# Kernel tuning notes

Measured on AMD Instinct MI355X. Metric: run time of the kernel, lower is better.

## Reference

```python
import jax, jax.numpy as jnp
import numpy as np

DIM = 1024
CTX_DIM = 1024
HEADS = 8
DIM_HEAD = 64
INNER = HEADS * DIM_HEAD  # 512
EPS = 1e-5


def _layer_norm(x, gamma, beta):
    mu = jnp.mean(x, axis=-1, keepdims=True)
    var = jnp.mean(jnp.square(x - mu), axis=-1, keepdims=True)
    return (x - mu) * jax.lax.rsqrt(var + EPS) * gamma + beta


def setup_inputs() -> dict:
    key = jax.random.key(0)
    ks = jax.random.split(key, 8)
    b, n, m = 4, 2048, 2048
    x = jax.random.normal(ks[0], (b, n, DIM), dtype=jnp.float32)
    context = jax.random.normal(ks[1], (b, m, CTX_DIM), dtype=jnp.float32)
    Wq = jax.random.normal(ks[2], (DIM, INNER), dtype=jnp.float32) / np.sqrt(DIM)
    Wkv = jax.random.normal(ks[3], (CTX_DIM, 2 * INNER), dtype=jnp.float32) / np.sqrt(CTX_DIM)
    Wout = jax.random.normal(ks[4], (INNER, DIM), dtype=jnp.float32) / np.sqrt(INNER)
    bout = jnp.zeros((DIM,), dtype=jnp.float32)
    g1 = jnp.ones((DIM,), dtype=jnp.float32)
    b1 = jnp.zeros((DIM,), dtype=jnp.float32)
    g2 = jnp.ones((CTX_DIM,), dtype=jnp.float32)
    b2 = jnp.zeros((CTX_DIM,), dtype=jnp.float32)
    return {"x": x, "context": context, "g1": g1, "b1": b1, "g2": g2, "b2": b2,
            "Wq": Wq, "Wkv": Wkv, "Wout": Wout, "bout": bout}


def reference(x, context, g1, b1, g2, b2, Wq, Wkv, Wout, bout):
    b, n, _ = x.shape
    m = context.shape[1]
    scale = DIM_HEAD ** -0.5
    xn = _layer_norm(x, g1, b1)
    cn = _layer_norm(context, g2, b2)
    q = xn @ Wq                      # [b, n, inner]
    kv = cn @ Wkv                    # [b, m, 2*inner]
    k, v = jnp.split(kv, 2, axis=-1)
    # split heads: [b, h, seq, d]
    q = q.reshape(b, n, HEADS, DIM_HEAD).transpose(0, 2, 1, 3)
    k = k.reshape(b, m, HEADS, DIM_HEAD).transpose(0, 2, 1, 3)
    v = v.reshape(b, m, HEADS, DIM_HEAD).transpose(0, 2, 1, 3)
    sim = jnp.einsum('bhid,bhjd->bhij', q, k) * scale
    attn = jax.nn.softmax(sim, axis=-1)
    out = jnp.einsum('bhij,bhjd->bhid', attn, v)
    out = out.transpose(0, 2, 1, 3).reshape(b, n, INNER)
    return out @ Wout + bout
```

## Files before the change

kernel.cpp:

```cpp
#include <hip/hip_runtime.h>
#include <hip/hip_bf16.h>

typedef __bf16 bf16_t;
typedef bf16_t bf16x4 __attribute__((ext_vector_type(4)));
typedef bf16_t bf16x8 __attribute__((ext_vector_type(8)));
typedef float floatx4 __attribute__((ext_vector_type(4)));

typedef __attribute__((address_space(1))) const unsigned char* gptr_t;
typedef __attribute__((address_space(3))) unsigned char* lptr_t;

#define BATCH 4
#define SEQ_N 2048
#define SEQ_M 2048
#define DIM 1024
#define INNER 512
#define HEADS 8
#define DHEAD 64
#define QSCALE 0.18033688011112042f

__device__ __forceinline__ void wtrans_tile(const float* W, bf16_t* Wt,
                                            int K, int N, int n0, int k0, float scale) {
    __shared__ bf16_t T[64][72];
    const int tid = threadIdx.x;
#pragma unroll
    for (int p = 0; p < 2; p++) {
        int r = (tid >> 3) + p * 32;
        int c = (tid & 7) * 8;
        const float* src = W + (size_t)(k0 + r) * N + n0 + c;
        float4 v0 = *(const float4*)src;
        float4 v1 = *(const float4*)(src + 4);
        T[r][c + 0] = (bf16_t)(v0.x * scale); T[r][c + 1] = (bf16_t)(v0.y * scale);
        T[r][c + 2] = (bf16_t)(v0.z * scale); T[r][c + 3] = (bf16_t)(v0.w * scale);
        T[r][c + 4] = (bf16_t)(v1.x * scale); T[r][c + 5] = (bf16_t)(v1.y * scale);
        T[r][c + 6] = (bf16_t)(v1.z * scale); T[r][c + 7] = (bf16_t)(v1.w * scale);
    }
    __syncthreads();
#pragma unroll
    for (int p = 0; p < 2; p++) {
        int rn = (tid >> 3) + p * 32;
        int ck = (tid & 7) * 8;
        bf16x8 v;
#pragma unroll
        for (int i = 0; i < 8; i++) v[i] = T[ck + i][rn];
        *(bf16x8*)(Wt + (size_t)(n0 + rn) * K + k0 + ck) = v;
    }
}

__device__ __forceinline__ void ln_row_wave(const float* in, const float* g,
                                            const float* bt, bf16_t* out, int row) {
    const int lane = threadIdx.x & 63;
    const float4* src = (const float4*)(in + (size_t)row * 1024);
    float4 xv[4];
    float s = 0.f, ss = 0.f;
#pragma unroll
    for (int k = 0; k < 4; k++) {
        xv[k] = src[lane + k * 64];
        s  += xv[k].x + xv[k].y + xv[k].z + xv[k].w;
        ss += xv[k].x * xv[k].x + xv[k].y * xv[k].y + xv[k].z * xv[k].z + xv[k].w * xv[k].w;
    }
#pragma unroll
    for (int off = 32; off > 0; off >>= 1) {
        s  += __shfl_down(s, off);
        ss += __shfl_down(ss, off);
    }
    s  = __shfl(s, 0);
    ss = __shfl(ss, 0);
    const float mu = s * (1.f / 1024.f);
    const float var = ss * (1.f / 1024.f) - mu * mu;
    const float rs = rsqrtf(var + 1e-5f);
    const float4* gp = (const float4*)g;
    const float4* bp = (const float4*)bt;
#pragma unroll
    for (int k = 0; k < 4; k++) {
        float4 gv = gp[lane + k * 64], bv = bp[lane + k * 64];
        bf16x4 o;
        o[0] = (bf16_t)((xv[k].x - mu) * rs * gv.x + bv.x);
        o[1] = (bf16_t)((xv[k].y - mu) * rs * gv.y + bv.y);
        o[2] = (bf16_t)((xv[k].z - mu) * rs * gv.z + bv.z);
        o[3] = (bf16_t)((xv[k].w - mu) * rs * gv.w + bv.w);
        *(bf16x4*)(out + (size_t)row * 1024 + (lane + k * 64) * 4) = o;
    }
}

__global__ __launch_bounds__(256) void prep_kernel(const float* __restrict__ x,
                                                   const float* __restrict__ ctx,
                                                   const float* __restrict__ g1,
                                                   const float* __restrict__ b1,
                                                   const float* __restrict__ g2,
                                                   const float* __restrict__ b2,
                                                   const float* __restrict__ Wq,
                                                   const float* __restrict__ Wkv,
                                                   const float* __restrict__ Wout,
                                                   bf16_t* __restrict__ xn,
                                                   bf16_t* __restrict__ cn,
                                                   bf16_t* __restrict__ Wqt,
                                                   bf16_t* __restrict__ Wkvt,
                                                   bf16_t* __restrict__ Woutt) {
    int id = blockIdx.x;
    if (id < 128) {
        wtrans_tile(Wq, Wqt, 1024, 512, (id & 7) * 64, (id >> 3) * 64, QSCALE);
    } else if (id < 384) {
        int t = id - 128;
        wtrans_tile(Wkv, Wkvt, 1024, 1024, (t & 15) * 64, (t >> 4) * 64, 1.0f);
    } else if (id < 512) {
        int t = id - 384;
        wtrans_tile(Wout, Woutt, 512, 1024, (t & 15) * 64, (t >> 4) * 64, 1.0f);
    } else {
        int row = (id - 512) * 4 + (threadIdx.x >> 6);
        if (row < BATCH * SEQ_N) ln_row_wave(x, g1, b1, xn, row);
        else                     ln_row_wave(ctx, g2, b2, cn, row - BATCH * SEQ_N);
    }
}

template <int NT, int MODE, typename OutT>
__device__ __forceinline__ void gemm_body(const bf16_t* __restrict__ A,
                                          const bf16_t* __restrict__ Bt,
                                          OutT* __restrict__ C,
                                          const float* __restrict__ bias,
                                          int ldC, int K, int row0, int col0) {
    __shared__ bf16_t As[128 * 64];
    __shared__ bf16_t Bs[NT * 64];
    const int tid = threadIdx.x;
    const int wave = tid >> 6, lane = tid & 63;
    constexpr int WC = NT / 2;
    constexpr int NJ = WC / 16;
    const int wr = (wave >> 1) * 64, wc = (wave & 1) * WC;
    const int quad = lane >> 4, l16 = lane & 15;

    floatx4 acc[4][NJ] = {};

    for (int k0 = 0; k0 < K; k0 += 64) {
#pragma unroll
        for (int p = 0; p < 4; p++) {
            int cA = p * 256 + wave * 64 + lane;
            int rA = cA >> 3, kc = (cA & 7) * 8;
            __builtin_amdgcn_global_load_lds(
                (gptr_t)(A + (size_t)(row0 + rA) * K + k0 + kc),
                (lptr_t)(As + (size_t)(p * 256 + wave * 64) * 8), 16, 0, 0);
            if (p < NT / 32)
                __builtin_amdgcn_global_load_lds(
                    (gptr_t)(Bt + (size_t)(col0 + rA) * K + k0 + kc),
                    (lptr_t)(Bs + (size_t)(p * 256 + wave * 64) * 8), 16, 0, 0);
        }
        __syncthreads();
#pragma unroll
        for (int kt = 0; kt < 2; kt++) {
            bf16x8 aF[4], bF[NJ];
#pragma unroll
            for (int i = 0; i < 4; i++)
                aF[i] = *(bf16x8*)&As[(wr + i * 16 + l16) * 64 + kt * 32 + quad * 8];
#pragma unroll
            for (int j = 0; j < NJ; j++)
                bF[j] = *(bf16x8*)&Bs[(wc + j * 16 + l16) * 64 + kt * 32 + quad * 8];
#pragma unroll
            for (int i = 0; i < 4; i++)
#pragma unroll
                for (int j = 0; j < NJ; j++) {
                    if (MODE == 0)
                        acc[i][j] = __builtin_amdgcn_mfma_f32_16x16x32_bf16(
                            aF[i], bF[j], acc[i][j], 0, 0, 0);
                    else
                        acc[i][j] = __builtin_amdgcn_mfma_f32_16x16x32_bf16(
                            bF[j], aF[i], acc[i][j], 0, 0, 0);
                }
        }
        __syncthreads();
    }

    if (MODE == 0) {
#pragma unroll
        for (int i = 0; i < 4; i++)
#pragma unroll
            for (int j = 0; j < NJ; j++) {
                int col = col0 + wc + j * 16 + l16;
                float bv = bias ? bias[col] : 0.f;
#pragma unroll
                for (int r = 0; r < 4; r++) {
                    int row = row0 + wr + i * 16 + quad * 4 + r;
                    C[(size_t)row * ldC + col] = (OutT)(acc[i][j][r] + bv);
                }
            }
    } else {
        bf16_t* Tw = (wave < 2 ? As : Bs) + (wave & 1) * 4096;
#pragma unroll
        for (int i = 0; i < 4; i++)
#pragma unroll
            for (int j = 0; j < 4; j++)
#pragma unroll
                for (int r = 0; r < 4; r++)
                    Tw[(j * 16 + quad * 4 + r) * 64 + i * 16 + l16] = (bf16_t)acc[i][j][r];
        __syncthreads();
        const int grow = row0 + wr;
        const int bat = grow >> 11, gm = (grow & 2047) + l16 * 4;
#pragma unroll
        for (int dd = 0; dd < 16; dd++) {
            int d = dd * 4 + quad;
            bf16x4 v = *(bf16x4*)&Tw[d * 64 + l16 * 4];
            int gd = col0 + wc + d - 512;
            *(bf16x4*)(C + ((size_t)bat * 512 + gd) * 2048 + gm) = v;
        }
    }
}

__global__ __launch_bounds__(256) void gemm_qkv_kernel(const bf16_t* __restrict__ xn,
                                                       const bf16_t* __restrict__ cn,
                                                       const bf16_t* __restrict__ Wqt,
                                                       const bf16_t* __restrict__ Wkvt,
                                                       bf16_t* __restrict__ qb,
                                                       bf16_t* __restrict__ kvb,
                                                       bf16_t* __restrict__ Vtg) {
    const int bx = blockIdx.x;
    const int row0 = blockIdx.y * 128;
    if (bx < 4)
        gemm_body<128, 0, bf16_t>(xn, Wqt, qb, nullptr, 512, DIM, row0, bx * 128);
    else if (bx < 8)
        gemm_body<128, 0, bf16_t>(cn, Wkvt, kvb, nullptr, 512, DIM, row0, (bx - 4) * 128);
    else
        gemm_body<128, 1, bf16_t>(cn, Wkvt, Vtg, nullptr, 0, DIM, row0, (bx - 4) * 128);
}

__global__ __launch_bounds__(256) void gemm_out_kernel(const bf16_t* __restrict__ ao,
                                                       const bf16_t* __restrict__ Woutt,
                                                       float* __restrict__ out,
                                                       const float* __restrict__ bias) {
    gemm_body<64, 0, float>(ao, Woutt, out, bias, DIM, INNER,
                            blockIdx.y * 128, blockIdx.x * 64);
}

#define PSTR 72
__global__ __launch_bounds__(256) void attn_kernel(const bf16_t* __restrict__ q,
                                                   const bf16_t* __restrict__ kv,
                                                   const bf16_t* __restrict__ Vtg,
                                                   bf16_t* __restrict__ o) {
    __shared__ bf16_t Qs[64 * 72];
    __shared__ bf16_t Ks[64 * 72];
    __shared__ bf16_t Vs[64 * 72];

    const int b = blockIdx.z, h = blockIdx.y;
    const int n0 = blockIdx.x * 64;
    const int tid = threadIdx.x;
    const int wave = tid >> 6, lane = tid & 63;
    const int quad = lane >> 4, l16 = lane & 15;

    const int sr = (tid >> 3);
    const int sc = (tid & 7) * 8;

#pragma unroll
    for (int p = 0; p < 2; p++) {
        int r = sr + p * 32;
        *(bf16x8*)&Qs[r * 72 + sc] =
            *(const bf16x8*)(q + (size_t)(b * SEQ_N + n0 + r) * INNER + h * DHEAD + sc);
    }

    bf16x8 bOnes;
    {
        bf16_t ov = (l16 == 0) ? (bf16_t)1.0f : (bf16_t)0.0f;
#pragma unroll
        for (int i = 0; i < 8; i++) bOnes[i] = ov;
    }

    const bf16_t* kp = kv + (size_t)(b * SEQ_M) * 512 + h * DHEAD + sc;
    const bf16_t* vp = Vtg + (size_t)((b * HEADS + h) * DHEAD) * SEQ_M + sc;
    bf16x8 kreg[2], vreg[2];
#pragma unroll
    for (int p = 0; p < 2; p++) {
        kreg[p] = *(const bf16x8*)(kp + (size_t)(sr + p * 32) * 512);
        vreg[p] = *(const bf16x8*)(vp + (size_t)(sr + p * 32) * SEQ_M);
    }
    __syncthreads();

    bf16x8 aQ[2];
#pragma unroll
    for (int kt = 0; kt < 2; kt++)
        aQ[kt] = *(bf16x8*)&Qs[(wave * 16 + l16) * 72 + kt * 32 + quad * 8];

    bf16_t* Pw = Qs + wave * (16 * PSTR);

    floatx4 oacc[5] = {};

    for (int it = 0; it < SEQ_M / 64; ++it) {
        __syncthreads();
#pragma unroll
        for (int p = 0; p < 2; p++) {
            int r = sr + p * 32;
            *(bf16x8*)&Ks[r * 72 + sc] = kreg[p];
            *(bf16x8*)&Vs[r * 72 + sc] = vreg[p];
        }
        __syncthreads();

        kp += 64 * 512;
        vp += 64;
#pragma unroll
        for (int p = 0; p < 2; p++) {
            kreg[p] = *(const bf16x8*)(kp + (size_t)(sr + p * 32) * 512);
            vreg[p] = *(const bf16x8*)(vp + (size_t)(sr + p * 32) * SEQ_M);
        }

        floatx4 s[4] = {};
#pragma unroll
        for (int kt = 0; kt < 2; kt++)
#pragma unroll
            for (int jt = 0; jt < 4; jt++) {
                bf16x8 aK = *(bf16x8*)&Ks[(jt * 16 + l16) * 72 + kt * 32 + quad * 8];
                s[jt] = __builtin_amdgcn_mfma_f32_16x16x32_bf16(aK, aQ[kt], s[jt], 0, 0, 0);
            }

#pragma unroll
        for (int jt = 0; jt < 4; jt++) {
            bf16x4 pk;
#pragma unroll
            for (int r = 0; r < 4; r++) pk[r] = (bf16_t)exp2f(s[jt][r]);
            *(bf16x4*)&Pw[l16 * PSTR + jt * 16 + quad * 4] = pk;
        }

#pragma unroll
        for (int kt = 0; kt < 2; kt++) {
            bf16x8 aP = *(bf16x8*)&Pw[l16 * PSTR + kt * 32 + quad * 8];
#pragma unroll
            for (int dt = 0; dt < 4; dt++) {
                bf16x8 bV = *(bf16x8*)&Vs[(dt * 16 + l16) * 72 + kt * 32 + quad * 8];
                oacc[dt] = __builtin_amdgcn_mfma_f32_16x16x32_bf16(aP, bV, oacc[dt], 0, 0, 0);
            }
            oacc[4] = __builtin_amdgcn_mfma_f32_16x16x32_bf16(aP, bOnes, oacc[4], 0, 0, 0);
        }
    }

    float inv[4];
#pragma unroll
    for (int r = 0; r < 4; r++) {
        float l = __shfl(oacc[4][r], (int)(lane & 48));
        inv[r] = 1.0f / l;
    }
#pragma unroll
    for (int dt = 0; dt < 4; dt++)
#pragma unroll
        for (int r = 0; r < 4; r++) {
            int row = n0 + wave * 16 + quad * 4 + r;
            int col = h * DHEAD + dt * 16 + l16;
            o[(size_t)(b * SEQ_N + row) * INNER + col] =
                (bf16_t)(oacc[dt][r] * inv[r]);
        }
}

extern "C" void kernel_launch(void* const* d_in, const int* in_sizes, int n_in,
                              void* d_out, int out_size, void* d_ws, size_t ws_size,
                              hipStream_t stream) {
    const float* x    = (const float*)d_in[0];
    const float* ctx  = (const float*)d_in[1];
    const float* g1   = (const float*)d_in[2];
    const float* b1   = (const float*)d_in[3];
    const float* g2   = (const float*)d_in[4];
    const float* b2   = (const float*)d_in[5];
    const float* Wq   = (const float*)d_in[6];
    const float* Wkv  = (const float*)d_in[7];
    const float* Wout = (const float*)d_in[8];
    const float* bout = (const float*)d_in[9];
    float* out = (float*)d_out;

    const int rows = BATCH * SEQ_N;
    bf16_t* xn    = (bf16_t*)d_ws;
    bf16_t* cn    = xn + (size_t)rows * DIM;
    bf16_t* qb    = cn + (size_t)rows * DIM;
    bf16_t* kvb   = qb + (size_t)rows * INNER;
    bf16_t* Vtg   = kvb + (size_t)rows * INNER;
    bf16_t* Wqt   = Vtg + (size_t)rows * INNER;
    bf16_t* Wkvt  = Wqt + (size_t)INNER * DIM;
    bf16_t* Woutt = Wkvt + (size_t)(2 * INNER) * DIM;
    bf16_t* o_attn = xn;

    prep_kernel<<<512 + (2 * rows) / 4, 256, 0, stream>>>(
        x, ctx, g1, b1, g2, b2, Wq, Wkv, Wout, xn, cn, Wqt, Wkvt, Woutt);
    gemm_qkv_kernel<<<dim3(12, rows / 128), 256, 0, stream>>>(
        xn, cn, Wqt, Wkvt, qb, kvb, Vtg);
    attn_kernel<<<dim3(SEQ_N / 64, HEADS, BATCH), 256, 0, stream>>>(qb, kvb, Vtg, o_attn);
    gemm_out_kernel<<<dim3(DIM / 64, rows / 128), 256, 0, stream>>>(o_attn, Woutt, out, bout);
}
```

Before: 259.9 us.

## Double-buffer K/V, process two query tiles per wave, swizzle LDS in attention

Result: no change. 257.4 us (-0.9%).

```diff
diff --git a/kernel.cpp b/kernel.cpp
--- a/kernel.cpp
+++ b/kernel.cpp
@@ -227,28 +227,32 @@
                             blockIdx.y * 128, blockIdx.x * 64);
 }
 
-#define PSTR 72
-__global__ __launch_bounds__(256) void attn_kernel(const bf16_t* __restrict__ q,
+__global__ __launch_bounds__(128) void attn_kernel(const bf16_t* __restrict__ q,
                                                    const bf16_t* __restrict__ kv,
                                                    const bf16_t* __restrict__ Vtg,
                                                    bf16_t* __restrict__ o) {
-    __shared__ bf16_t Qs[64 * 72];
-    __shared__ bf16_t Ks[64 * 72];
-    __shared__ bf16_t Vs[64 * 72];
-
-    const int b = blockIdx.z, h = blockIdx.y;
-    const int n0 = blockIdx.x * 64;
+    __shared__ bf16_t Qs[64 * 64];
+    __shared__ bf16_t Ks[2][64 * 64];
+    __shared__ bf16_t Vs[2][64 * 64];
+
+    const int f = blockIdx.x;
+    const int lb = ((f & 7) << 7) | (f >> 3);
+    const int b = lb >> 8, h = (lb >> 5) & 7;
+    const int n0 = (lb & 31) * 64;
+
     const int tid = threadIdx.x;
     const int wave = tid >> 6, lane = tid & 63;
     const int quad = lane >> 4, l16 = lane & 15;
-
-    const int sr = (tid >> 3);
+    const int swz = (l16 & 7) << 3;
+
+    const int sr = tid >> 3;
     const int sc = (tid & 7) * 8;
-
-#pragma unroll
-    for (int p = 0; p < 2; p++) {
-        int r = sr + p * 32;
-        *(bf16x8*)&Qs[r * 72 + sc] =
+    const int scs = sc ^ ((sr & 7) << 3);
+
+#pragma unroll
+    for (int p = 0; p < 4; p++) {
+        int r = sr + p * 16;
+        *(bf16x8*)&Qs[r * 64 + scs] =
             *(const bf16x8*)(q + (size_t)(b * SEQ_N + n0 + r) * INNER + h * DHEAD + sc);
     }
 
@@ -261,85 +265,118 @@
 
     const bf16_t* kp = kv + (size_t)(b * SEQ_M) * 512 + h * DHEAD + sc;
     const bf16_t* vp = Vtg + (size_t)((b * HEADS + h) * DHEAD) * SEQ_M + sc;
-    bf16x8 kreg[2], vreg[2];
-#pragma unroll
-    for (int p = 0; p < 2; p++) {
-        kreg[p] = *(const bf16x8*)(kp + (size_t)(sr + p * 32) * 512);
-        vreg[p] = *(const bf16x8*)(vp + (size_t)(sr + p * 32) * SEQ_M);
+    bf16x8 kreg[4], vreg[4];
+#pragma unroll
+    for (int p = 0; p < 4; p++) {
+        kreg[p] = *(const bf16x8*)(kp + (size_t)(sr + p * 16) * 512);
+        vreg[p] = *(const bf16x8*)(vp + (size_t)(sr + p * 16) * SEQ_M);
     }
     __syncthreads();
 
-    bf16x8 aQ[2];
-#pragma unroll
-    for (int kt = 0; kt < 2; kt++)
-        aQ[kt] = *(bf16x8*)&Qs[(wave * 16 + l16) * 72 + kt * 32 + quad * 8];
-
-    bf16_t* Pw = Qs + wave * (16 * PSTR);
-
-    floatx4 oacc[5] = {};
-
+    bf16x8 aQ0[2], aQ1[2];
+#pragma unroll
+    for (int kt = 0; kt < 2; kt++) {
+        aQ0[kt] = *(bf16x8*)&Qs[(wave * 32 + l16) * 64 + ((kt * 32 + quad * 8) ^ swz)];
+        aQ1[kt] = *(bf16x8*)&Qs[(wave * 32 + 16 + l16) * 64 + ((kt * 32 + quad * 8) ^ swz)];
+    }
+
+#pragma unroll
+    for (int p = 0; p < 4; p++) {
+        int r = sr + p * 16;
+        *(bf16x8*)&Ks[0][r * 64 + scs] = kreg[p];
+        *(bf16x8*)&Vs[0][r * 64 + scs] = vreg[p];
+    }
+    kp += 64 * 512;
+    vp += 64;
+#pragma unroll
+    for (int p = 0; p < 4; p++) {
+        kreg[p] = *(const bf16x8*)(kp + (size_t)(sr + p * 16) * 512);
+        vreg[p] = *(const bf16x8*)(vp + (size_t)(sr + p * 16) * SEQ_M);
+    }
+    __syncthreads();
+
+    bf16_t* Pw0 = Qs + wave * 2048;
+    bf16_t* Pw1 = Pw0 + 1024;
+
+    floatx4 oacc0[5] = {}, oacc1[5] = {};
+
+    int cur = 0;
     for (int it = 0; it < SEQ_M / 64; ++it) {
-        __syncthreads();
-#pragma unroll
-        for (int p = 0; p < 2; p++) {
-            int r = sr + p * 32;
-            *(bf16x8*)&Ks[r * 72 + sc] = kreg[p];
-            *(bf16x8*)&Vs[r * 72 + sc] = vreg[p];
-        }
-        __syncthreads();
-
+#pragma unroll
+        for (int p = 0; p < 4; p++) {
+            int r = sr + p * 16;
+            *(bf16x8*)&Ks[cur ^ 1][r * 64 + scs] = kreg[p];
+            *(bf16x8*)&Vs[cur ^ 1][r * 64 + scs] = vreg[p];
+        }
         kp += 64 * 512;
         vp += 64;
 #pragma unroll
-        for (int p = 0; p < 2; p++) {
-            kreg[p] = *(const bf16x8*)(kp + (size_t)(sr + p * 32) * 512);
-            vreg[p] = *(const bf16x8*)(vp + (size_t)(sr + p * 32) * SEQ_M);
-        }
-
-        floatx4 s[4] = {};
+        for (int p = 0; p < 4; p++) {
+            kreg[p] = *(const bf16x8*)(kp + (size_t)(sr + p * 16) * 512);
+            vreg[p] = *(const bf16x8*)(vp + (size_t)(sr + p * 16) * SEQ_M);
+        }
+
+        floatx4 s0[4] = {}, s1[4] = {};
 #pragma unroll
         for (int kt = 0; kt < 2; kt++)
 #pragma unroll
             for (int jt = 0; jt < 4; jt++) {
-                bf16x8 aK = *(bf16x8*)&Ks[(jt * 16 + l16) * 72 + kt * 32 + quad * 8];
-                s[jt] = __builtin_amdgcn_mfma_f32_16x16x32_bf16(aK, aQ[kt], s[jt], 0, 0, 0);
+                bf16x8 aK = *(bf16x8*)&Ks[cur][(jt * 16 + l16) * 64 +
+                                              ((kt * 32 + quad * 8) ^ swz)];
+                s0[jt] = __builtin_amdgcn_mfma_f32_16x16x32_bf16(aK, aQ0[kt], s0[jt], 0, 0, 0);
+                s1[jt] = __builtin_amdgcn_mfma_f32_16x16x32_bf16(aK, aQ1[kt], s1[jt], 0, 0, 0);
             }
 
 #pragma unroll
         for (int jt = 0; jt < 4; jt++) {
-            bf16x4 pk;
-#pragma unroll
-            for (int r = 0; r < 4; r++) pk[r] = (bf16_t)exp2f(s[jt][r]);
-            *(bf16x4*)&Pw[l16 * PSTR + jt * 16 + quad * 4] = pk;
+            bf16x4 pk0, pk1;
+#pragma unroll
+            for (int r = 0; r < 4; r++) {
+                pk0[r] = (bf16_t)exp2f(s0[jt][r]);
+                pk1[r] = (bf16_t)exp2f(s1[jt][r]);
+            }
+            int pc = (jt * 16 + quad * 4) ^ swz;
+            *(bf16x4*)&Pw0[l16 * 64 + pc] = pk0;
+            *(bf16x4*)&Pw1[l16 * 64 + pc] = pk1;
         }
 
 #pragma unroll
         for (int kt = 0; kt < 2; kt++) {
-            bf16x8 aP = *(bf16x8*)&Pw[l16 * PSTR + kt * 32 + quad * 8];
+            int ac = (kt * 32 + quad * 8) ^ swz;
+            bf16x8 aP0 = *(bf16x8*)&Pw0[l16 * 64 + ac];
+            bf16x8 aP1 = *(bf16x8*)&Pw1[l16 * 64 + ac];
 #pragma unroll
             for (int dt = 0; dt < 4; dt++) {
-                bf16x8 bV = *(bf16x8*)&Vs[(dt * 16 + l16) * 72 + kt * 32 + quad * 8];
-                oacc[dt] = __builtin_amdgcn_mfma_f32_16x16x32_bf16(aP, bV, oacc[dt], 0, 0, 0);
+                bf16x8 bV = *(bf16x8*)&Vs[cur][(dt * 16 + l16) * 64 + ac];
+                oacc0[dt] = __builtin_amdgcn_mfma_f32_16x16x32_bf16(aP0, bV, oacc0[dt], 0, 0, 0);
+                oacc1[dt] = __builtin_amdgcn_mfma_f32_16x16x32_bf16(aP1, bV, oacc1[dt], 0, 0, 0);
             }
-            oacc[4] = __builtin_amdgcn_mfma_f32_16x16x32_bf16(aP, bOnes, oacc[4], 0, 0, 0);
-        }
-    }
-
-    float inv[4];
-#pragma unroll
-    for (int r = 0; r < 4; r++) {
-        float l = __shfl(oacc[4][r], (int)(lane & 48));
-        inv[r] = 1.0f / l;
-    }
-#pragma unroll
-    for (int dt = 0; dt < 4; dt++)
+            oacc0[4] = __builtin_amdgcn_mfma_f32_16x16x32_bf16(aP0, bOnes, oacc0[4], 0, 0, 0);
+            oacc1[4] = __builtin_amdgcn_mfma_f32_16x16x32_bf16(aP1, bOnes, oacc1[4], 0, 0, 0);
+        }
+        __syncthreads();
+        cur ^= 1;
+    }
+
+#pragma unroll
+    for (int set = 0; set < 2; set++) {
+        const floatx4* oa = set == 0 ? oacc0 : oacc1;
+        float inv[4];
 #pragma unroll
         for (int r = 0; r < 4; r++) {
-            int row = n0 + wave * 16 + quad * 4 + r;
-            int col = h * DHEAD + dt * 16 + l16;
-            o[(size_t)(b * SEQ_N + row) * INNER + col] =
-                (bf16_t)(oacc[dt][r] * inv[r]);
-        }
+            float l = __shfl(oa[4][r], (int)(lane & 48));
+            inv[r] = 1.0f / l;
+        }
+#pragma unroll
+        for (int dt = 0; dt < 4; dt++)
+#pragma unroll
+            for (int r = 0; r < 4; r++) {
+                int row = n0 + wave * 32 + set * 16 + quad * 4 + r;
+                int col = h * DHEAD + dt * 16 + l16;
+                o[(size_t)(b * SEQ_N + row) * INNER + col] =
+                    (bf16_t)(oa[dt][r] * inv[r]);
+            }
+    }
 }
 
 extern "C" void kernel_launch(void* const* d_in, const int* in_sizes, int n_in,
@@ -372,6 +409,6 @@
         x, ctx, g1, b1, g2, b2, Wq, Wkv, Wout, xn, cn, Wqt, Wkvt, Woutt);
     gemm_qkv_kernel<<<dim3(12, rows / 128), 256, 0, stream>>>(
         xn, cn, Wqt, Wkvt, qb, kvb, Vtg);
-    attn_kernel<<<dim3(SEQ_N / 64, HEADS, BATCH), 256, 0, stream>>>(qb, kvb, Vtg, o_attn);
+    attn_kernel<<<dim3(SEQ_N / 64 * HEADS * BATCH), 128, 0, stream>>>(qb, kvb, Vtg, o_attn);
     gemm_out_kernel<<<dim3(DIM / 64, rows / 128), 256, 0, stream>>>(o_attn, Woutt, out, bout);
 }
```

## Load K/V fragments directly to registers and process 32 query rows per wave

Applied to the files above, without the earlier changes.

Result: slower. 307.1 us (+18.2%).

```diff
diff --git a/kernel.cpp b/kernel.cpp
--- a/kernel.cpp
+++ b/kernel.cpp
@@ -17,6 +17,12 @@
 #define HEADS 8
 #define DHEAD 64
 #define QSCALE 0.18033688011112042f
+
+#if __has_builtin(__builtin_amdgcn_exp2f)
+#define fast_exp2(x) __builtin_amdgcn_exp2f(x)
+#else
+#define fast_exp2(x) exp2f(x)
+#endif
 
 __device__ __forceinline__ void wtrans_tile(const float* W, bf16_t* Wt,
                                             int K, int N, int n0, int k0, float scale) {
@@ -227,29 +233,33 @@
                             blockIdx.y * 128, blockIdx.x * 64);
 }
 
-#define PSTR 72
-__global__ __launch_bounds__(256) void attn_kernel(const bf16_t* __restrict__ q,
-                                                   const bf16_t* __restrict__ kv,
-                                                   const bf16_t* __restrict__ Vtg,
-                                                   bf16_t* __restrict__ o) {
-    __shared__ bf16_t Qs[64 * 72];
-    __shared__ bf16_t Ks[64 * 72];
-    __shared__ bf16_t Vs[64 * 72];
-
-    const int b = blockIdx.z, h = blockIdx.y;
-    const int n0 = blockIdx.x * 64;
+__global__ __launch_bounds__(256, 2) void attn_kernel(const bf16_t* __restrict__ q,
+                                                      const bf16_t* __restrict__ kv,
+                                                      const bf16_t* __restrict__ Vtg,
+                                                      bf16_t* __restrict__ o) {
+    __shared__ bf16_t Ps[4][2048];
+
+    const int f = blockIdx.x;
+    const int lb = ((f & 7) << 6) | (f >> 3);
+    const int b = lb >> 7, h = (lb >> 4) & 7;
+    const int n0 = (lb & 15) * 128;
+
     const int tid = threadIdx.x;
     const int wave = tid >> 6, lane = tid & 63;
     const int quad = lane >> 4, l16 = lane & 15;
-
-    const int sr = (tid >> 3);
-    const int sc = (tid & 7) * 8;
-
-#pragma unroll
-    for (int p = 0; p < 2; p++) {
-        int r = sr + p * 32;
-        *(bf16x8*)&Qs[r * 72 + sc] =
-            *(const bf16x8*)(q + (size_t)(b * SEQ_N + n0 + r) * INNER + h * DHEAD + sc);
+    const int swz = (l16 & 7) << 3;
+
+    const int qrow = n0 + wave * 32;
+
+    bf16x8 aQ[2][2];
+    {
+        const bf16_t* qbase =
+            q + (size_t)(b * SEQ_N + qrow + l16) * INNER + h * DHEAD + quad * 8;
+#pragma unroll
+        for (int set = 0; set < 2; set++)
+#pragma unroll
+            for (int kt = 0; kt < 2; kt++)
+                aQ[set][kt] = *(const bf16x8*)(qbase + set * 16 * INNER + kt * 32);
     }
 
     bf16x8 bOnes;
@@ -259,87 +269,95 @@
         for (int i = 0; i < 8; i++) bOnes[i] = ov;
     }
 
-    const bf16_t* kp = kv + (size_t)(b * SEQ_M) * 512 + h * DHEAD + sc;
-    const bf16_t* vp = Vtg + (size_t)((b * HEADS + h) * DHEAD) * SEQ_M + sc;
-    bf16x8 kreg[2], vreg[2];
-#pragma unroll
-    for (int p = 0; p < 2; p++) {
-        kreg[p] = *(const bf16x8*)(kp + (size_t)(sr + p * 32) * 512);
-        vreg[p] = *(const bf16x8*)(vp + (size_t)(sr + p * 32) * SEQ_M);
-    }
-    __syncthreads();
-
-    bf16x8 aQ[2];
-#pragma unroll
-    for (int kt = 0; kt < 2; kt++)
-        aQ[kt] = *(bf16x8*)&Qs[(wave * 16 + l16) * 72 + kt * 32 + quad * 8];
-
-    bf16_t* Pw = Qs + wave * (16 * PSTR);
-
-    floatx4 oacc[5] = {};
+    const bf16_t* kb = kv + (size_t)(b * SEQ_M + l16) * 512 + h * DHEAD + quad * 8;
+    const bf16_t* vb =
+        Vtg + ((size_t)((b * HEADS + h) * DHEAD) + l16) * SEQ_M + quad * 8;
+
+    bf16x8 kf[2][4], vf[2][4];
+#pragma unroll
+    for (int jt = 0; jt < 4; jt++)
+#pragma unroll
+        for (int kt = 0; kt < 2; kt++) {
+            kf[kt][jt] = *(const bf16x8*)(kb + (size_t)(jt * 16) * 512 + kt * 32);
+            vf[kt][jt] = *(const bf16x8*)(vb + (size_t)(jt * 16) * SEQ_M + kt * 32);
+        }
+
+    bf16_t* Pw = Ps[wave];
+    floatx4 oacc[2][5] = {};
 
     for (int it = 0; it < SEQ_M / 64; ++it) {
-        __syncthreads();
-#pragma unroll
-        for (int p = 0; p < 2; p++) {
-            int r = sr + p * 32;
-            *(bf16x8*)&Ks[r * 72 + sc] = kreg[p];
-            *(bf16x8*)&Vs[r * 72 + sc] = vreg[p];
-        }
-        __syncthreads();
-
-        kp += 64 * 512;
-        vp += 64;
-#pragma unroll
-        for (int p = 0; p < 2; p++) {
-            kreg[p] = *(const bf16x8*)(kp + (size_t)(sr + p * 32) * 512);
-            vreg[p] = *(const bf16x8*)(vp + (size_t)(sr + p * 32) * SEQ_M);
-        }
-
-        floatx4 s[4] = {};
+        floatx4 s[2][4] = {};
 #pragma unroll
         for (int kt = 0; kt < 2; kt++)
 #pragma unroll
             for (int jt = 0; jt < 4; jt++) {
-                bf16x8 aK = *(bf16x8*)&Ks[(jt * 16 + l16) * 72 + kt * 32 + quad * 8];
-                s[jt] = __builtin_amdgcn_mfma_f32_16x16x32_bf16(aK, aQ[kt], s[jt], 0, 0, 0);
-            }
-
-#pragma unroll
-        for (int jt = 0; jt < 4; jt++) {
-            bf16x4 pk;
-#pragma unroll
-            for (int r = 0; r < 4; r++) pk[r] = (bf16_t)exp2f(s[jt][r]);
-            *(bf16x4*)&Pw[l16 * PSTR + jt * 16 + quad * 4] = pk;
-        }
+                s[0][jt] = __builtin_amdgcn_mfma_f32_16x16x32_bf16(
+                    kf[kt][jt], aQ[0][kt], s[0][jt], 0, 0, 0);
+                s[1][jt] = __builtin_amdgcn_mfma_f32_16x16x32_bf16(
+                    kf[kt][jt], aQ[1][kt], s[1][jt], 0, 0, 0);
+            }
+
+        kb += 64 * 512;
+#pragma unroll
+        for (int jt = 0; jt < 4; jt++)
+#pragma unroll
+            for (int kt = 0; kt < 2; kt++)
+                kf[kt][jt] = *(const bf16x8*)(kb + (size_t)(jt * 16) * 512 + kt * 32);
+
+#pragma unroll
+        for (int set = 0; set < 2; set++)
+#pragma unroll
+            for (int jt = 0; jt < 4; jt++) {
+                bf16x4 pk;
+#pragma unroll
+                for (int r = 0; r < 4; r++) pk[r] = (bf16_t)fast_exp2(s[set][jt][r]);
+                *(bf16x4*)&Pw[(set * 16 + l16) * 64 + ((jt * 16 + quad * 4) ^ swz)] = pk;
+            }
 
 #pragma unroll
         for (int kt = 0; kt < 2; kt++) {
-            bf16x8 aP = *(bf16x8*)&Pw[l16 * PSTR + kt * 32 + quad * 8];
+            int ac = (kt * 32 + quad * 8) ^ swz;
+            bf16x8 aP0 = *(bf16x8*)&Pw[l16 * 64 + ac];
+            bf16x8 aP1 = *(bf16x8*)&Pw[1024 + l16 * 64 + ac];
 #pragma unroll
             for (int dt = 0; dt < 4; dt++) {
-                bf16x8 bV = *(bf16x8*)&Vs[(dt * 16 + l16) * 72 + kt * 32 + quad * 8];
-                oacc[dt] = __builtin_amdgcn_mfma_f32_16x16x32_bf16(aP, bV, oacc[dt], 0, 0, 0);
-            }
-            oacc[4] = __builtin_amdgcn_mfma_f32_16x16x32_bf16(aP, bOnes, oacc[4], 0, 0, 0);
-        }
-    }
-
-    float inv[4];
-#pragma unroll
-    for (int r = 0; r < 4; r++) {
-        float l = __shfl(oacc[4][r], (int)(lane & 48));
-        inv[r] = 1.0f / l;
-    }
-#pragma unroll
-    for (int dt = 0; dt < 4; dt++)
+                oacc[0][dt] = __builtin_amdgcn_mfma_f32_16x16x32_bf16(
+                    aP0, vf[kt][dt], oacc[0][dt], 0, 0, 0);
+                oacc[1][dt] = __builtin_amdgcn_mfma_f32_16x16x32_bf16(
+                    aP1, vf[kt][dt], oacc[1][dt], 0, 0, 0);
+            }
+            oacc[0][4] = __builtin_amdgcn_mfma_f32_16x16x32_bf16(
+                aP0, bOnes, oacc[0][4], 0, 0, 0);
+            oacc[1][4] = __builtin_amdgcn_mfma_f32_16x16x32_bf16(
+                aP1, bOnes, oacc[1][4], 0, 0, 0);
+        }
+
+        vb += 64;
+#pragma unroll
+        for (int dt = 0; dt < 4; dt++)
+#pragma unroll
+            for (int kt = 0; kt < 2; kt++)
+                vf[kt][dt] = *(const bf16x8*)(vb + (size_t)(dt * 16) * SEQ_M + kt * 32);
+    }
+
+#pragma unroll
+    for (int set = 0; set < 2; set++) {
+        float inv[4];
 #pragma unroll
         for (int r = 0; r < 4; r++) {
-            int row = n0 + wave * 16 + quad * 4 + r;
-            int col = h * DHEAD + dt * 16 + l16;
-            o[(size_t)(b * SEQ_N + row) * INNER + col] =
-                (bf16_t)(oacc[dt][r] * inv[r]);
-        }
+            float l = __shfl(oacc[set][4][r], (int)(lane & 48));
+            inv[r] = 1.0f / l;
+        }
+#pragma unroll
+        for (int dt = 0; dt < 4; dt++)
+#pragma unroll
+            for (int r = 0; r < 4; r++) {
+                int row = n0 + wave * 32 + set * 16 + quad * 4 + r;
+                int col = h * DHEAD + dt * 16 + l16;
+                o[(size_t)(b * SEQ_N + row) * INNER + col] =
+                    (bf16_t)(oacc[set][dt][r] * inv[r]);
+            }
+    }
 }
 
 extern "C" void kernel_launch(void* const* d_in, const int* in_sizes, int n_in,
@@ -372,6 +390,6 @@
         x, ctx, g1, b1, g2, b2, Wq, Wkv, Wout, xn, cn, Wqt, Wkvt, Woutt);
     gemm_qkv_kernel<<<dim3(12, rows / 128), 256, 0, stream>>>(
         xn, cn, Wqt, Wkvt, qb, kvb, Vtg);
-    attn_kernel<<<dim3(SEQ_N / 64, HEADS, BATCH), 256, 0, stream>>>(qb, kvb, Vtg, o_attn);
+    attn_kernel<<<dim3(SEQ_N / 128 * HEADS * BATCH), 256, 0, stream>>>(qb, kvb, Vtg, o_attn);
     gemm_out_kernel<<<dim3(DIM / 64, rows / 128), 256, 0, stream>>>(o_attn, Woutt, out, bout);
 }
```
